# Kernel tuning notes

Hardware: AMD Instinct MI355X
Metric: run time of the kernel (lower is better)

The kernel has to match this reference:

```python
import jax, jax.numpy as jnp
import numpy as np

BS, Z, NOBJ = 16384, 512, 64


def setup_inputs() -> dict:
    key = jax.random.key(0)
    ks = jax.random.split(key, 12)
    din = Z + 4  # z concatenated with bounds (x_size = 0)

    def lin(k, i, o):
        kw, kb = jax.random.split(k)
        w = jax.random.normal(kw, (i, o), jnp.float32) * (1.0 / np.sqrt(i))
        b = jax.random.normal(kb, (o,), jnp.float32) * 0.01
        return w, b

    W1, c1 = lin(ks[0], din, 512)
    W2, c2 = lin(ks[1], 512, 256)
    W3, c3 = lin(ks[2], 256, 128)
    W4, c4 = lin(ks[3], 128, 64)
    W5, c5 = lin(ks[4], 64, NOBJ * 4)
    z = jax.random.normal(ks[5], (BS, Z), jnp.float32)
    # room bounds [x_min, y_min, x_max, y_max]; must allow gaps >= 1
    bounds = jnp.array([0.0, 0.0, 40.0, 40.0], jnp.float32)
    return {"z": z, "bounds": bounds,
            "W1": W1, "c1": c1, "W2": W2, "c2": c2, "W3": W3, "c3": c3,
            "W4": W4, "c4": c4, "W5": W5, "c5": c5}


def _lrelu(v):
    return jnp.where(v > 0, v, 0.2 * v)


def _solve_axis(pp, pg, lo, hi):
    """Exact KKT solution of: min (x-pp)^2 + (g-pg)^2  s.t. x>=lo, g>=1, x+g<=hi.
    Returns (x, w) with w = x + g. Matches the parabolic QP per object/axis."""
    x0 = jnp.maximum(pp, lo)          # box projection (lower bounds only)
    g0 = jnp.maximum(pg, 1.0)
    t = 0.5 * (hi - pp - pg)          # projection of (pp,pg) onto line x+g=hi
    xl = jnp.clip(pp + t, lo, hi - 1.0)
    over = (x0 + g0) > hi             # coupling constraint active?
    x = jnp.where(over, xl, x0)
    g = jnp.where(over, hi - xl, g0)
    return x, x + g


def reference(z, bounds, W1, c1, W2, c2, W3, c3, W4, c4, W5, c5):
    bs = z.shape[0]
    bnd = jnp.broadcast_to(bounds, (bs, 4))
    h = jnp.concatenate([z, bnd], axis=1)          # (bs, z_size+4)
    h = _lrelu(h @ W1 + c1)                        # dropout treated as eval/identity
    h = _lrelu(h @ W2 + c2)
    h = _lrelu(h @ W3 + c3)
    h = _lrelu(h @ W4 + c4)
    p = (h @ W5 + c5).reshape(bs, NOBJ, 4)         # per-object params [px, py, pw, ph]
    px, py, pw, ph = p[..., 0], p[..., 1], p[..., 2], p[..., 3]
    b0, b1, b2, b3 = bounds[0], bounds[1], bounds[2], bounds[3]
    # QP objective: sum (x-px)^2+(y-py)^2+((w-x)-pw)^2+((h-y)-ph)^2
    # s.t. x>=b0, y>=b1, w<=b2, h<=b3, x<=w-1, y<=h-1. Separable per object/axis.
    xs, ws = _solve_axis(px, pw, b0, b2)
    ys, hs = _solve_axis(py, ph, b1, b3)
    return jnp.stack([xs, ys, ws, hs], axis=-1)    # (bs, num_objs, 4)
```

## Files before the change

### kernel.cpp

```cpp
#include <hip/hip_runtime.h>


#define MROWS 16384

typedef __attribute__((ext_vector_type(8))) short bf16x8;
typedef __attribute__((ext_vector_type(4))) float floatx4;

__device__ __forceinline__ unsigned short f2bf(float x) {
    union { float f; unsigned u; } c; c.f = x;
    unsigned r = c.u + 0x7fffu + ((c.u >> 16) & 1u);
    return (unsigned short)(r >> 16);
}
__device__ __forceinline__ float bf2f(unsigned short b) {
    union { unsigned u; float f; } c; c.u = ((unsigned)b) << 16;
    return c.f;
}

__global__ __launch_bounds__(256) void pack_wt(
    const float* __restrict__ W1, unsigned short* __restrict__ T1,
    const float* __restrict__ W2, unsigned short* __restrict__ T2,
    const float* __restrict__ W3, unsigned short* __restrict__ T3,
    const float* __restrict__ W4, unsigned short* __restrict__ T4,
    const float* __restrict__ W5, unsigned short* __restrict__ T5h,
    unsigned short* __restrict__ T5l)
{
    const int idx = blockIdx.x * 256 + threadIdx.x;
    if (blockIdx.y == 4) {
        if (idx >= 256 * 64) return;
        const int k = idx >> 8, n = idx & 255;
        const float v = W5[idx];
        const unsigned short hi = f2bf(v);
        const unsigned short lo = f2bf(v - bf2f(hi));
        const int ntile = n >> 4, m_l = n & 15;
        const int ks = k >> 5, quad = (k >> 3) & 3, e = k & 7;
        const size_t o = (size_t)(((ntile * 2 + ks) * 64) + quad * 16 + m_l) * 8 + e;
        T5h[o] = hi; T5l[o] = lo;
        return;
    }
    const float* W; unsigned short* T; int Kreal, KS, nshift;
    switch (blockIdx.y) {
        case 0:  W = W1; T = T1; Kreal = 516; KS = 17; nshift = 9; break;
        case 1:  W = W2; T = T2; Kreal = 512; KS = 16; nshift = 8; break;
        case 2:  W = W3; T = T3; Kreal = 256; KS = 8;  nshift = 7; break;
        default: W = W4; T = T4; Kreal = 128; KS = 4;  nshift = 6; break;
    }
    const int N = 1 << nshift;
    if (idx >= N * KS * 32) return;
    const int k = idx >> nshift;
    const int n = idx & (N - 1);
    const unsigned short v = (k < Kreal) ? f2bf(W[idx]) : (unsigned short)0;
    const int ntile = n >> 4, m_l = n & 15;
    const int ks = k >> 5, quad = (k >> 3) & 3, e = k & 7;
    T[(size_t)(((ntile * KS + ks) * 64) + quad * 16 + m_l) * 8 + e] = v;
}

#define OFF_ZS   0
#define LD_ZS    552
#define OFF_H1   17664
#define LD_H1    520
#define OFF_H2   0
#define LD_H2    264
#define OFF_H3   17664
#define LD_H3    136
#define OFF_H4   8448
#define LD_H4    72
#define OFF_P    17664
#define LD_P     260
#define LDS_TOT  34304

template<int NF, int KSTEPS>
__device__ __forceinline__ void layer_gemm(
    unsigned short* lds, int offA, int lda, int offC, int ldc,
    const unsigned short* __restrict__ Wt,
    const float* __restrict__ bias, int wid, int lane)
{
    const int m_l = lane & 15, quad = lane >> 4;
    const unsigned short* __restrict__ Wl =
        Wt + ((size_t)(wid * NF) * KSTEPS * 64 + lane) * 8;
    floatx4 acc[2][NF];
    #pragma unroll
    for (int i = 0; i < 2; ++i)
        #pragma unroll
        for (int j = 0; j < NF; ++j)
            acc[i][j] = (floatx4){0.f, 0.f, 0.f, 0.f};

    #pragma unroll
    for (int ks = 0; ks < KSTEPS; ++ks) {
        const bf16x8 a0 = *(const bf16x8*)&lds[offA + (m_l     ) * lda + ks*32 + quad*8];
        const bf16x8 a1 = *(const bf16x8*)&lds[offA + (m_l + 16) * lda + ks*32 + quad*8];
        #pragma unroll
        for (int j = 0; j < NF; ++j) {
            const bf16x8 b = *(const bf16x8*)(Wl + (size_t)(j * KSTEPS + ks) * 512);
            acc[0][j] = __builtin_amdgcn_mfma_f32_16x16x32_bf16(a0, b, acc[0][j], 0, 0, 0);
            acc[1][j] = __builtin_amdgcn_mfma_f32_16x16x32_bf16(a1, b, acc[1][j], 0, 0, 0);
        }
    }
    #pragma unroll
    for (int j = 0; j < NF; ++j) {
        const int col = wid * (NF * 16) + j * 16 + m_l;
        const float bv = bias[col];
        #pragma unroll
        for (int i = 0; i < 2; ++i)
            #pragma unroll
            for (int r = 0; r < 4; ++r) {
                float v = acc[i][j][r] + bv;
                v = v > 0.f ? v : 0.2f * v;
                lds[offC + (i*16 + quad*4 + r) * ldc + col] = f2bf(v);
            }
    }
}

__global__ __launch_bounds__(256, 2) void fused_mlp_qp(
    const float* __restrict__ z, const float* __restrict__ bounds,
    const unsigned short* __restrict__ Wt1, const float* __restrict__ c1,
    const unsigned short* __restrict__ Wt2, const float* __restrict__ c2,
    const unsigned short* __restrict__ Wt3, const float* __restrict__ c3,
    const unsigned short* __restrict__ Wt4, const float* __restrict__ c4,
    const unsigned short* __restrict__ Wt5h, const unsigned short* __restrict__ Wt5l,
    const float* __restrict__ c5,
    float* __restrict__ out)
{
    __shared__ unsigned short lds[LDS_TOT];
    const int tid  = threadIdx.x;
    const int wid  = tid >> 6, lane = tid & 63;
    const int m_l  = lane & 15, quad = lane >> 4;
    const int bm   = blockIdx.x * 32;

    const float4 bnd = *(const float4*)bounds;

    {
        const float4* __restrict__ zf = (const float4*)(z + (size_t)bm * 512);
        #pragma unroll
        for (int i = 0; i < 16; ++i) {
            const int f   = i * 256 + tid;
            const int row = f >> 7, c4i = f & 127;
            const float4 v = zf[f];
            unsigned short t4[4] = {f2bf(v.x), f2bf(v.y), f2bf(v.z), f2bf(v.w)};
            *(uint2*)&lds[OFF_ZS + row * LD_ZS + c4i * 4] = *(uint2*)t4;
        }
        if (tid < 160) {
            const int row = tid / 5, j = tid % 5;
            unsigned short t8[8] = {0,0,0,0,0,0,0,0};
            if (j == 0) { t8[0] = f2bf(bnd.x); t8[1] = f2bf(bnd.y);
                          t8[2] = f2bf(bnd.z); t8[3] = f2bf(bnd.w); }
            *(uint4*)&lds[OFF_ZS + row * LD_ZS + 512 + j * 8] = *(uint4*)t8;
        }
    }
    __syncthreads();

    layer_gemm<8,17>(lds, OFF_ZS, LD_ZS, OFF_H1, LD_H1, Wt1, c1, wid, lane);
    __syncthreads();
    layer_gemm<4,16>(lds, OFF_H1, LD_H1, OFF_H2, LD_H2, Wt2, c2, wid, lane);
    __syncthreads();
    layer_gemm<2,8 >(lds, OFF_H2, LD_H2, OFF_H3, LD_H3, Wt3, c3, wid, lane);
    __syncthreads();
    layer_gemm<1,4 >(lds, OFF_H3, LD_H3, OFF_H4, LD_H4, Wt4, c4, wid, lane);
    __syncthreads();

    {
        const size_t wb = ((size_t)(wid * 4) * 2 * 64 + lane) * 8;
        const unsigned short* __restrict__ Wh = Wt5h + wb;
        const unsigned short* __restrict__ Wl = Wt5l + wb;
        floatx4 acc[2][4];
        #pragma unroll
        for (int i = 0; i < 2; ++i)
            #pragma unroll
            for (int j = 0; j < 4; ++j) acc[i][j] = (floatx4){0.f,0.f,0.f,0.f};

        #pragma unroll
        for (int ks = 0; ks < 2; ++ks) {
            const bf16x8 a0 = *(const bf16x8*)&lds[OFF_H4 + (m_l     ) * LD_H4 + ks*32 + quad*8];
            const bf16x8 a1 = *(const bf16x8*)&lds[OFF_H4 + (m_l + 16) * LD_H4 + ks*32 + quad*8];
            #pragma unroll
            for (int j = 0; j < 4; ++j) {
                const bf16x8 bh = *(const bf16x8*)(Wh + (size_t)(j * 2 + ks) * 512);
                const bf16x8 bl = *(const bf16x8*)(Wl + (size_t)(j * 2 + ks) * 512);
                acc[0][j] = __builtin_amdgcn_mfma_f32_16x16x32_bf16(a0, bh, acc[0][j], 0, 0, 0);
                acc[0][j] = __builtin_amdgcn_mfma_f32_16x16x32_bf16(a0, bl, acc[0][j], 0, 0, 0);
                acc[1][j] = __builtin_amdgcn_mfma_f32_16x16x32_bf16(a1, bh, acc[1][j], 0, 0, 0);
                acc[1][j] = __builtin_amdgcn_mfma_f32_16x16x32_bf16(a1, bl, acc[1][j], 0, 0, 0);
            }
        }
        float* __restrict__ p = (float*)&lds[OFF_P];
        #pragma unroll
        for (int j = 0; j < 4; ++j) {
            const int col = wid * 64 + j * 16 + m_l;
            const float bv = c5[col];
            #pragma unroll
            for (int i = 0; i < 2; ++i)
                #pragma unroll
                for (int r = 0; r < 4; ++r)
                    p[(i*16 + quad*4 + r) * LD_P + col] = acc[i][j][r] + bv;
        }
    }
    __syncthreads();

    const float b0 = bnd.x, b1 = bnd.y, b2 = bnd.z, b3 = bnd.w;
    const float* __restrict__ p = (const float*)&lds[OFF_P];
    #pragma unroll
    for (int i = 0; i < 8; ++i) {
        const int row = i * 4 + wid;
        const float4 pv = *(const float4*)&p[row * LD_P + lane * 4];
        float xs, wo, ys, ho;
        {
            const float px = pv.x, pw = pv.z;
            const float x0 = fmaxf(px, b0);
            const float g0 = fmaxf(pw, 1.0f);
            const float t  = 0.5f * (b2 - px - pw);
            const float xl = fminf(fmaxf(px + t, b0), b2 - 1.0f);
            const bool over = (x0 + g0) > b2;
            const float x = over ? xl : x0;
            const float g = over ? (b2 - xl) : g0;
            xs = x; wo = x + g;
        }
        {
            const float py = pv.y, ph = pv.w;
            const float x0 = fmaxf(py, b1);
            const float g0 = fmaxf(ph, 1.0f);
            const float t  = 0.5f * (b3 - py - ph);
            const float xl = fminf(fmaxf(py + t, b1), b3 - 1.0f);
            const bool over = (x0 + g0) > b3;
            const float x = over ? xl : x0;
            const float g = over ? (b3 - xl) : g0;
            ys = x; ho = x + g;
        }
        float4 o; o.x = xs; o.y = ys; o.z = wo; o.w = ho;
        ((float4*)out)[(size_t)(bm + row) * 64 + lane] = o;
    }
}

extern "C" void kernel_launch(void* const* d_in, const int* in_sizes, int n_in,
                              void* d_out, int out_size, void* d_ws, size_t ws_size,
                              hipStream_t stream) {
    const float* z      = (const float*)d_in[0];
    const float* bounds = (const float*)d_in[1];
    const float* W1 = (const float*)d_in[2];
    const float* c1 = (const float*)d_in[3];
    const float* W2 = (const float*)d_in[4];
    const float* c2 = (const float*)d_in[5];
    const float* W3 = (const float*)d_in[6];
    const float* c3 = (const float*)d_in[7];
    const float* W4 = (const float*)d_in[8];
    const float* c4 = (const float*)d_in[9];
    const float* W5 = (const float*)d_in[10];
    const float* c5 = (const float*)d_in[11];
    float* out = (float*)d_out;

    unsigned short* ws   = (unsigned short*)d_ws;
    unsigned short* Wt1  = ws;
    unsigned short* Wt2  = Wt1 + 278528;
    unsigned short* Wt3  = Wt2 + 131072;
    unsigned short* Wt4  = Wt3 + 32768;
    unsigned short* Wt5h = Wt4 + 8192;
    unsigned short* Wt5l = Wt5h + 16384;

    pack_wt<<<dim3(1088, 5), 256, 0, stream>>>(
        W1, Wt1, W2, Wt2, W3, Wt3, W4, Wt4, W5, Wt5h, Wt5l);
    fused_mlp_qp<<<dim3(MROWS / 32), 256, 0, stream>>>(
        z, bounds, Wt1, c1, Wt2, c2, Wt3, c3, Wt4, c4, Wt5h, Wt5l, c5, out);
}
```

Baseline: 128.7 us.

## Stream weight fragments through a register ring with inline-asm loads and waits

Reorders the packed weight layout to be k-step-major and interleaves the hi/lo split of W5, then has each layer prefetch weight fragments into a ring of up to 8 registers. It uses inline-asm global loads and explicit vmcnt waits so that MFMAs overlap with outstanding weight loads. Bias is folded into the accumulator initialisation. The aim is to hide global/L2 latency on weight fetches. The cost is more VGPRs under launch bounds of 2 blocks, plus redundant dummy loads at the ring tail.

After: 124.3 us. 3.4% less time.

```diff
diff --git a/kernel.cpp b/kernel.cpp
--- a/kernel.cpp
+++ b/kernel.cpp
@@ -14,6 +14,30 @@
 __device__ __forceinline__ float bf2f(unsigned short b) {
     union { unsigned u; float f; } c; c.u = ((unsigned)b) << 16;
     return c.f;
+}
+
+__device__ __forceinline__ bf16x8 gload(const unsigned short* p) {
+    bf16x8 r;
+    asm volatile("global_load_dwordx4 %0, %1, off"
+                 : "=&v"(r)
+                 : "v"((unsigned long long)(size_t)p)
+                 : "memory");
+    return r;
+}
+template<int IMM>
+__device__ __forceinline__ void vwait(bf16x8& v) {
+    asm volatile("s_waitcnt vmcnt(%1)" : "+v"(v) : "n"(IMM) : "memory");
+}
+__device__ __forceinline__ void drain8(bf16x8 (&r)[8]) {
+    asm volatile("s_waitcnt vmcnt(0)"
+                 : "+v"(r[0]), "+v"(r[1]), "+v"(r[2]), "+v"(r[3]),
+                   "+v"(r[4]), "+v"(r[5]), "+v"(r[6]), "+v"(r[7])
+                 :: "memory");
+}
+__device__ __forceinline__ void drain4(bf16x8 (&r)[4]) {
+    asm volatile("s_waitcnt vmcnt(0)"
+                 : "+v"(r[0]), "+v"(r[1]), "+v"(r[2]), "+v"(r[3])
+                 :: "memory");
 }
 
 __global__ __launch_bounds__(256) void pack_wt(
@@ -21,8 +45,7 @@
     const float* __restrict__ W2, unsigned short* __restrict__ T2,
     const float* __restrict__ W3, unsigned short* __restrict__ T3,
     const float* __restrict__ W4, unsigned short* __restrict__ T4,
-    const float* __restrict__ W5, unsigned short* __restrict__ T5h,
-    unsigned short* __restrict__ T5l)
+    const float* __restrict__ W5, unsigned short* __restrict__ T5)
 {
     const int idx = blockIdx.x * 256 + threadIdx.x;
     if (blockIdx.y == 4) {
@@ -33,25 +56,26 @@
         const unsigned short lo = f2bf(v - bf2f(hi));
         const int ntile = n >> 4, m_l = n & 15;
         const int ks = k >> 5, quad = (k >> 3) & 3, e = k & 7;
-        const size_t o = (size_t)(((ntile * 2 + ks) * 64) + quad * 16 + m_l) * 8 + e;
-        T5h[o] = hi; T5l[o] = lo;
+        const size_t b = (size_t)(((ks * 16 + ntile) * 2) * 64 + quad * 16 + m_l) * 8 + e;
+        T5[b] = hi; T5[b + 512] = lo;
         return;
     }
-    const float* W; unsigned short* T; int Kreal, KS, nshift;
+    const float* W; unsigned short* T; int Kreal, nshift;
     switch (blockIdx.y) {
-        case 0:  W = W1; T = T1; Kreal = 516; KS = 17; nshift = 9; break;
-        case 1:  W = W2; T = T2; Kreal = 512; KS = 16; nshift = 8; break;
-        case 2:  W = W3; T = T3; Kreal = 256; KS = 8;  nshift = 7; break;
-        default: W = W4; T = T4; Kreal = 128; KS = 4;  nshift = 6; break;
-    }
-    const int N = 1 << nshift;
+        case 0:  W = W1; T = T1; Kreal = 516; nshift = 9; break;
+        case 1:  W = W2; T = T2; Kreal = 512; nshift = 8; break;
+        case 2:  W = W3; T = T3; Kreal = 256; nshift = 7; break;
+        default: W = W4; T = T4; Kreal = 128; nshift = 6; break;
+    }
+    const int N = 1 << nshift, NT = N >> 4;
+    const int KS = (Kreal + 31) >> 5;
     if (idx >= N * KS * 32) return;
     const int k = idx >> nshift;
     const int n = idx & (N - 1);
     const unsigned short v = (k < Kreal) ? f2bf(W[idx]) : (unsigned short)0;
     const int ntile = n >> 4, m_l = n & 15;
     const int ks = k >> 5, quad = (k >> 3) & 3, e = k & 7;
-    T[(size_t)(((ntile * KS + ks) * 64) + quad * 16 + m_l) * 8 + e] = v;
+    T[(size_t)((ks * NT + ntile) * 64 + quad * 16 + m_l) * 8 + e] = v;
 }
 
 #define OFF_ZS   0
@@ -68,42 +92,54 @@
 #define LD_P     260
 #define LDS_TOT  34304
 
-template<int NF, int KSTEPS>
-__device__ __forceinline__ void layer_gemm(
+template<int NF, int KSTEPS, int NT, int DEP>
+__device__ __forceinline__ void layer_stream(
     unsigned short* lds, int offA, int lda, int offC, int ldc,
     const unsigned short* __restrict__ Wt,
     const float* __restrict__ bias, int wid, int lane)
 {
     const int m_l = lane & 15, quad = lane >> 4;
-    const unsigned short* __restrict__ Wl =
-        Wt + ((size_t)(wid * NF) * KSTEPS * 64 + lane) * 8;
+    constexpr int NFR = NF * KSTEPS;
+    const unsigned short* __restrict__ Wb = Wt + ((size_t)(wid * NF) * 64 + lane) * 8;
+
     floatx4 acc[2][NF];
     #pragma unroll
-    for (int i = 0; i < 2; ++i)
-        #pragma unroll
-        for (int j = 0; j < NF; ++j)
-            acc[i][j] = (floatx4){0.f, 0.f, 0.f, 0.f};
-
-    #pragma unroll
-    for (int ks = 0; ks < KSTEPS; ++ks) {
-        const bf16x8 a0 = *(const bf16x8*)&lds[offA + (m_l     ) * lda + ks*32 + quad*8];
-        const bf16x8 a1 = *(const bf16x8*)&lds[offA + (m_l + 16) * lda + ks*32 + quad*8];
-        #pragma unroll
-        for (int j = 0; j < NF; ++j) {
-            const bf16x8 b = *(const bf16x8*)(Wl + (size_t)(j * KSTEPS + ks) * 512);
-            acc[0][j] = __builtin_amdgcn_mfma_f32_16x16x32_bf16(a0, b, acc[0][j], 0, 0, 0);
-            acc[1][j] = __builtin_amdgcn_mfma_f32_16x16x32_bf16(a1, b, acc[1][j], 0, 0, 0);
-        }
-    }
+    for (int j = 0; j < NF; ++j) {
+        const float bv = bias[wid * (NF * 16) + j * 16 + m_l];
+        acc[0][j] = (floatx4){bv, bv, bv, bv};
+        acc[1][j] = (floatx4){bv, bv, bv, bv};
+    }
+
+    bf16x8 ring[DEP];
+    #pragma unroll
+    for (int f = 0; f < DEP; ++f) {
+        const int g = (f < NFR) ? f : 0;
+        ring[f] = gload(Wb + (size_t)((g / NF) * NT + (g % NF)) * 512);
+    }
+    bf16x8 a0, a1;
+    #pragma unroll
+    for (int f = 0; f < NFR; ++f) {
+        const int ks = f / NF, j = f - ks * NF;
+        if (j == 0) {
+            a0 = *(const bf16x8*)&lds[offA + (m_l     ) * lda + ks*32 + quad*8];
+            a1 = *(const bf16x8*)&lds[offA + (m_l + 16) * lda + ks*32 + quad*8];
+        }
+        vwait<DEP - 1>(ring[f % DEP]);
+        acc[0][j] = __builtin_amdgcn_mfma_f32_16x16x32_bf16(a0, ring[f % DEP], acc[0][j], 0, 0, 0);
+        acc[1][j] = __builtin_amdgcn_mfma_f32_16x16x32_bf16(a1, ring[f % DEP], acc[1][j], 0, 0, 0);
+        const int nf2 = (f + DEP < NFR) ? f + DEP : 0;
+        ring[f % DEP] = gload(Wb + (size_t)((nf2 / NF) * NT + (nf2 % NF)) * 512);
+    }
+    if constexpr (DEP == 8) drain8(ring); else drain4(ring);
+
     #pragma unroll
     for (int j = 0; j < NF; ++j) {
         const int col = wid * (NF * 16) + j * 16 + m_l;
-        const float bv = bias[col];
         #pragma unroll
         for (int i = 0; i < 2; ++i)
             #pragma unroll
             for (int r = 0; r < 4; ++r) {
-                float v = acc[i][j][r] + bv;
+                float v = acc[i][j][r];
                 v = v > 0.f ? v : 0.2f * v;
                 lds[offC + (i*16 + quad*4 + r) * ldc + col] = f2bf(v);
             }
@@ -116,8 +152,7 @@
     const unsigned short* __restrict__ Wt2, const float* __restrict__ c2,
     const unsigned short* __restrict__ Wt3, const float* __restrict__ c3,
     const unsigned short* __restrict__ Wt4, const float* __restrict__ c4,
-    const unsigned short* __restrict__ Wt5h, const unsigned short* __restrict__ Wt5l,
-    const float* __restrict__ c5,
+    const unsigned short* __restrict__ Wt5, const float* __restrict__ c5,
     float* __restrict__ out)
 {
     __shared__ unsigned short lds[LDS_TOT];
@@ -148,49 +183,56 @@
     }
     __syncthreads();
 
-    layer_gemm<8,17>(lds, OFF_ZS, LD_ZS, OFF_H1, LD_H1, Wt1, c1, wid, lane);
-    __syncthreads();
-    layer_gemm<4,16>(lds, OFF_H1, LD_H1, OFF_H2, LD_H2, Wt2, c2, wid, lane);
-    __syncthreads();
-    layer_gemm<2,8 >(lds, OFF_H2, LD_H2, OFF_H3, LD_H3, Wt3, c3, wid, lane);
-    __syncthreads();
-    layer_gemm<1,4 >(lds, OFF_H3, LD_H3, OFF_H4, LD_H4, Wt4, c4, wid, lane);
+    layer_stream<8,17,32,8>(lds, OFF_ZS, LD_ZS, OFF_H1, LD_H1, Wt1, c1, wid, lane);
+    __syncthreads();
+    layer_stream<4,16,16,8>(lds, OFF_H1, LD_H1, OFF_H2, LD_H2, Wt2, c2, wid, lane);
+    __syncthreads();
+    layer_stream<2,8, 8, 8>(lds, OFF_H2, LD_H2, OFF_H3, LD_H3, Wt3, c3, wid, lane);
+    __syncthreads();
+    layer_stream<1,4, 4, 4>(lds, OFF_H3, LD_H3, OFF_H4, LD_H4, Wt4, c4, wid, lane);
     __syncthreads();
 
     {
-        const size_t wb = ((size_t)(wid * 4) * 2 * 64 + lane) * 8;
-        const unsigned short* __restrict__ Wh = Wt5h + wb;
-        const unsigned short* __restrict__ Wl = Wt5l + wb;
+        const unsigned short* __restrict__ Wb5 = Wt5 + (size_t)wid * 4096 + (size_t)lane * 8;
         floatx4 acc[2][4];
         #pragma unroll
-        for (int i = 0; i < 2; ++i)
-            #pragma unroll
-            for (int j = 0; j < 4; ++j) acc[i][j] = (floatx4){0.f,0.f,0.f,0.f};
-
-        #pragma unroll
-        for (int ks = 0; ks < 2; ++ks) {
-            const bf16x8 a0 = *(const bf16x8*)&lds[OFF_H4 + (m_l     ) * LD_H4 + ks*32 + quad*8];
-            const bf16x8 a1 = *(const bf16x8*)&lds[OFF_H4 + (m_l + 16) * LD_H4 + ks*32 + quad*8];
-            #pragma unroll
-            for (int j = 0; j < 4; ++j) {
-                const bf16x8 bh = *(const bf16x8*)(Wh + (size_t)(j * 2 + ks) * 512);
-                const bf16x8 bl = *(const bf16x8*)(Wl + (size_t)(j * 2 + ks) * 512);
-                acc[0][j] = __builtin_amdgcn_mfma_f32_16x16x32_bf16(a0, bh, acc[0][j], 0, 0, 0);
-                acc[0][j] = __builtin_amdgcn_mfma_f32_16x16x32_bf16(a0, bl, acc[0][j], 0, 0, 0);
-                acc[1][j] = __builtin_amdgcn_mfma_f32_16x16x32_bf16(a1, bh, acc[1][j], 0, 0, 0);
-                acc[1][j] = __builtin_amdgcn_mfma_f32_16x16x32_bf16(a1, bl, acc[1][j], 0, 0, 0);
+        for (int j = 0; j < 4; ++j) {
+            const float bv = c5[wid * 64 + j * 16 + m_l];
+            acc[0][j] = (floatx4){bv, bv, bv, bv};
+            acc[1][j] = (floatx4){bv, bv, bv, bv};
+        }
+        auto w5off = [](int g) {
+            const int ks = g >> 3, rem = g & 7;
+            return (size_t)ks * 16384 + (size_t)(rem >> 1) * 1024 + (size_t)(rem & 1) * 512;
+        };
+        bf16x8 ring[8];
+        #pragma unroll
+        for (int f = 0; f < 8; ++f) ring[f] = gload(Wb5 + w5off(f));
+        bf16x8 a0, a1;
+        #pragma unroll
+        for (int f = 0; f < 16; ++f) {
+            const int ks = f >> 3, rem = f & 7, j = rem >> 1;
+            if (rem == 0) {
+                a0 = *(const bf16x8*)&lds[OFF_H4 + (m_l     ) * LD_H4 + ks*32 + quad*8];
+                a1 = *(const bf16x8*)&lds[OFF_H4 + (m_l + 16) * LD_H4 + ks*32 + quad*8];
             }
-        }
+            vwait<7>(ring[f & 7]);
+            acc[0][j] = __builtin_amdgcn_mfma_f32_16x16x32_bf16(a0, ring[f & 7], acc[0][j], 0, 0, 0);
+            acc[1][j] = __builtin_amdgcn_mfma_f32_16x16x32_bf16(a1, ring[f & 7], acc[1][j], 0, 0, 0);
+            const int nf2 = (f + 8 < 16) ? f + 8 : 0;
+            ring[f & 7] = gload(Wb5 + w5off(nf2));
+        }
+        drain8(ring);
+
         float* __restrict__ p = (float*)&lds[OFF_P];
         #pragma unroll
         for (int j = 0; j < 4; ++j) {
             const int col = wid * 64 + j * 16 + m_l;
-            const float bv = c5[col];
             #pragma unroll
             for (int i = 0; i < 2; ++i)
                 #pragma unroll
                 for (int r = 0; r < 4; ++r)
-                    p[(i*16 + quad*4 + r) * LD_P + col] = acc[i][j][r] + bv;
+                    p[(i*16 + quad*4 + r) * LD_P + col] = acc[i][j][r];
         }
     }
     __syncthreads();
@@ -246,16 +288,15 @@
     const float* c5 = (const float*)d_in[11];
     float* out = (float*)d_out;
 
-    unsigned short* ws   = (unsigned short*)d_ws;
-    unsigned short* Wt1  = ws;
-    unsigned short* Wt2  = Wt1 + 278528;
-    unsigned short* Wt3  = Wt2 + 131072;
-    unsigned short* Wt4  = Wt3 + 32768;
-    unsigned short* Wt5h = Wt4 + 8192;
-    unsigned short* Wt5l = Wt5h + 16384;
+    unsigned short* ws  = (unsigned short*)d_ws;
+    unsigned short* Wt1 = ws;
+    unsigned short* Wt2 = Wt1 + 278528;
+    unsigned short* Wt3 = Wt2 + 131072;
+    unsigned short* Wt4 = Wt3 + 32768;
+    unsigned short* Wt5 = Wt4 + 8192;
 
     pack_wt<<<dim3(1088, 5), 256, 0, stream>>>(
-        W1, Wt1, W2, Wt2, W3, Wt3, W4, Wt4, W5, Wt5h, Wt5l);
+        W1, Wt1, W2, Wt2, W3, Wt3, W4, Wt4, W5, Wt5);
     fused_mlp_qp<<<dim3(MROWS / 32), 256, 0, stream>>>(
-        z, bounds, Wt1, c1, Wt2, c2, Wt3, c3, Wt4, c4, Wt5h, Wt5l, c5, out);
-}
+        z, bounds, Wt1, c1, Wt2, c2, Wt3, c3, Wt4, c4, Wt5, c5, out);
+}
```
